# Optimization experiments

Hardware: AMD Instinct MI355X
Metric: run time of the kernel (lower is better)

## Reference

```python
import jax, jax.numpy as jnp
import numpy as np

N = 50000   # nodes
R = 3       # relations
E = 300000  # edges per relation
H, D = 4, 32  # heads, per-head dim (hidden_feat=128)
IN, HID, OUT = 128, 128, 64
SLOPE = 0.2  # DGL GATConv leaky_relu negative slope


def setup_inputs() -> dict:
    key = jax.random.key(0)
    ks = jax.random.split(key, 12)
    s = 0.05
    return {
        "x": jax.random.normal(ks[0], (N, IN), jnp.float32),
        "edges": jax.random.randint(ks[1], (R, 2, E), 0, N, jnp.int64),
        "W1": jax.random.normal(ks[2], (R, IN, H * D), jnp.float32) * s,
        "al1": jax.random.normal(ks[3], (R, H, D), jnp.float32) * s,
        "ar1": jax.random.normal(ks[4], (R, H, D), jnp.float32) * s,
        "b1": jnp.zeros((R, H, D), jnp.float32),
        "W2": jax.random.normal(ks[5], (R, HID, H * D), jnp.float32) * s,
        "al2": jax.random.normal(ks[6], (R, H, D), jnp.float32) * s,
        "ar2": jax.random.normal(ks[7], (R, H, D), jnp.float32) * s,
        "b2": jnp.zeros((R, H, D), jnp.float32),
        "Wl": jax.random.normal(ks[8], (HID, OUT), jnp.float32) * s,
        "bl": jnp.zeros((OUT,), jnp.float32),
    }


def rgat_layer(h, edges, W, al, ar, b):
    """HeteroGraphConv(sum) of per-relation GATConv. h: [N,F]. Returns [N,H,D]."""
    out = jnp.zeros((N, H, D), h.dtype)
    for r in range(R):  # small fixed relation count
        src, dst = edges[r, 0], edges[r, 1]
        feat = (h @ W[r]).reshape(N, H, D)                  # per-relation projection
        el = jnp.einsum("nhd,hd->nh", feat, al[r])          # [N,H]
        er = jnp.einsum("nhd,hd->nh", feat, ar[r])          # [N,H]
        e = jax.nn.leaky_relu(el[src] + er[dst], SLOPE)      # [E,H]
        # edge softmax over incoming edges per destination node
        emax = jax.ops.segment_max(e, dst, num_segments=N)   # [N,H]
        ex = jnp.exp(e - emax[dst])
        denom = jax.ops.segment_sum(ex, dst, num_segments=N) # [N,H]
        alpha = ex / denom[dst]                               # [E,H]
        msg = feat[src] * alpha[:, :, None]                   # [E,H,D]
        out = out + jax.ops.segment_sum(msg, dst, num_segments=N) + b[r]
    return out


def reference(x, edges, W1, al1, ar1, b1, W2, al2, ar2, b2, Wl, bl):
    h = rgat_layer(x, edges, W1, al1, ar1, b1).reshape(N, H * D)
    h = jax.nn.relu(h)  # dropout is identity in eval mode
    h = rgat_layer(h, edges, W2, al2, ar2, b2).reshape(N, H * D)
    return h @ Wl + bl  # [N, OUT]
```

## Files before the change

### kernel.cpp

```cpp
#include <hip/hip_runtime.h>
#include <hip/hip_bf16.h>
#include <hip/hip_fp16.h>
#include <type_traits>

#define Nn 50000
#define RR 3
#define EE 300000

typedef __attribute__((ext_vector_type(8))) short short8;
typedef __attribute__((ext_vector_type(4))) short short4v;
typedef __attribute__((ext_vector_type(4))) float floatx4;

__device__ __forceinline__ short f2bf(float f) {
    __hip_bfloat16 h = __float2bfloat16(f);
    return *reinterpret_cast<short*>(&h);
}


__global__ void count_wswz_kernel(const int* __restrict__ edges, int* __restrict__ counts,
                                  int* __restrict__ ord,
                                  const float* __restrict__ W1, const float* __restrict__ W2,
                                  short* __restrict__ Z) {
    int bx = blockIdx.x;
    if (bx >= 440) {
        int idx = (bx - 440) * 256 + threadIdx.x;
        if (idx >= 12288) return;
        int lane = idx & 63;
        int nt = (idx >> 6) & 7;
        int kt = (idx >> 9) & 3;
        int rl = idx >> 11;
        int layer = rl / 3, r = rl % 3;
        const float* W = (layer ? W2 : W1) + (size_t)r * 16384;
        int n = nt * 16 + (lane & 15);
        int k0 = kt * 32 + (lane >> 4) * 8;
        short8 v;
        #pragma unroll
        for (int j = 0; j < 8; ++j) v[j] = f2bf(W[(size_t)(k0 + j) * 128 + n]);
        *(short8*)&Z[(size_t)idx * 8] = v;
        return;
    }
    int i = bx * 256 + threadIdx.x;
    if (i >= RR * EE / 8) return;
    int g = i * 8;
    int r = g / EE, e0 = g - r * EE;
    const int* db = &edges[(size_t)r * 2 * EE + EE + e0];
    int4 d0 = *(const int4*)db;
    int4 d1 = *(const int4*)(db + 4);
    int* cb = counts + r * Nn;
    int4 o0, o1;
    o0.x = atomicAdd(&cb[d0.x], 1);
    o0.y = atomicAdd(&cb[d0.y], 1);
    o0.z = atomicAdd(&cb[d0.z], 1);
    o0.w = atomicAdd(&cb[d0.w], 1);
    o1.x = atomicAdd(&cb[d1.x], 1);
    o1.y = atomicAdd(&cb[d1.y], 1);
    o1.z = atomicAdd(&cb[d1.z], 1);
    o1.w = atomicAdd(&cb[d1.w], 1);
    *(int4*)&ord[g] = o0;
    *(int4*)&ord[g + 4] = o1;
}

__global__ __launch_bounds__(256) void alloc_kernel(const int* __restrict__ counts,
                                                    int* __restrict__ row_start,
                                                    int* __restrict__ totals) {
    __shared__ int s[256];
    __shared__ int base_s;
    int r = blockIdx.y;
    int tid = threadIdx.x;
    int n = blockIdx.x * 256 + tid;
    int idx = r * Nn + n;
    int c = (n < Nn) ? counts[idx] : 0;
    s[tid] = c;
    __syncthreads();
    #pragma unroll
    for (int off = 1; off < 256; off <<= 1) {
        int v = 0;
        if (tid >= off) v = s[tid - off];
        __syncthreads();
        if (tid >= off) s[tid] += v;
        __syncthreads();
    }
    if (tid == 255) base_s = atomicAdd(&totals[r], s[255]);
    __syncthreads();
    if (n < Nn) row_start[idx] = base_s + s[tid] - c;
}


__device__ __forceinline__ void scatter_body(int bid, const int* __restrict__ edges,
                                             const int* __restrict__ ord,
                                             const int* __restrict__ row_start,
                                             int* __restrict__ csr_s, int* __restrict__ csr_d) {
    int i = bid * 256 + threadIdx.x;
    if (i >= RR * EE / 8) return;
    int g = i * 8;
    int r = g / EE, e0 = g - r * EE;
    const int* sb = &edges[(size_t)r * 2 * EE + e0];
    const int* db = sb + EE;
    int4 s0 = *(const int4*)sb, s1 = *(const int4*)(sb + 4);
    int4 d0 = *(const int4*)db, d1 = *(const int4*)(db + 4);
    int4 o0 = *(const int4*)&ord[g], o1 = *(const int4*)&ord[g + 4];
    const int* rs = row_start + r * Nn;
    int* cs = csr_s + (size_t)r * EE;
    int* cd = csr_d + (size_t)r * EE;
    int p0 = rs[d0.x] + o0.x, p1 = rs[d0.y] + o0.y;
    int p2 = rs[d0.z] + o0.z, p3 = rs[d0.w] + o0.w;
    int p4 = rs[d1.x] + o1.x, p5 = rs[d1.y] + o1.y;
    int p6 = rs[d1.z] + o1.z, p7 = rs[d1.w] + o1.w;
    cs[p0] = s0.x; cs[p1] = s0.y; cs[p2] = s0.z; cs[p3] = s0.w;
    cs[p4] = s1.x; cs[p5] = s1.y; cs[p6] = s1.z; cs[p7] = s1.w;
    cd[p0] = d0.x; cd[p1] = d0.y; cd[p2] = d0.z; cd[p3] = d0.w;
    cd[p4] = d1.x; cd[p5] = d1.y; cd[p6] = d1.z; cd[p7] = d1.w;
}


template<typename TA, bool FUSE_SCATTER>
__global__ __launch_bounds__(256) void gemm_proj_mfma(const TA* __restrict__ A,
                                                      const short* __restrict__ Z,
                                                      const float* __restrict__ al,
                                                      const float* __restrict__ ar,
                                                      __half* __restrict__ C,
                                                      float* __restrict__ el,
                                                      float* __restrict__ er,
                                                      const int* __restrict__ edges,
                                                      const int* __restrict__ ord,
                                                      const int* __restrict__ row_start,
                                                      int* __restrict__ csr_s,
                                                      int* __restrict__ csr_d) {
    const int rowBlocks = (Nn + 63) / 64;
    if (FUSE_SCATTER && blockIdx.x >= rowBlocks) {
        scatter_body(blockIdx.x - rowBlocks, edges, ord, row_start, csr_s, csr_d);
        return;
    }
    __shared__ short A_lds[64 * 136];
    __shared__ float al_lds[384], ar_lds[384];
    int tid = threadIdx.x;
    int row0 = blockIdx.x * 64;
    if (tid < 128) { al_lds[256 + tid] = al[256 + tid]; ar_lds[256 + tid] = ar[256 + tid]; }
    al_lds[tid] = al[tid]; ar_lds[tid] = ar[tid];
    if constexpr (std::is_same<TA, float>::value) {
        #pragma unroll
        for (int p = 0; p < 8; ++p) {
            int f = p * 256 + tid;
            int row = f >> 5;
            int c4 = (f & 31) * 4;
            float4 v = make_float4(0.f, 0.f, 0.f, 0.f);
            if (row0 + row < Nn) v = *(const float4*)&A[(size_t)(row0 + row) * 128 + c4];
            short4v sv;
            sv[0] = f2bf(v.x); sv[1] = f2bf(v.y); sv[2] = f2bf(v.z); sv[3] = f2bf(v.w);
            *(short4v*)&A_lds[row * 136 + c4] = sv;
        }
    } else {
        #pragma unroll
        for (int p = 0; p < 4; ++p) {
            int c = p * 256 + tid;
            int row = c >> 4, c8 = (c & 15) * 8;
            short8 v = (short8)(0);
            if (row0 + row < Nn) v = *(const short8*)&A[(size_t)(row0 + row) * 128 + c8];
            *(short8*)&A_lds[row * 136 + c8] = v;
        }
    }
    __syncthreads();
    int wave = tid >> 6, lane = tid & 63;
    int m = lane & 15, q = lane >> 4;
    short8 af[4];
    #pragma unroll
    for (int kt = 0; kt < 4; ++kt)
        af[kt] = *(short8*)&A_lds[(wave * 16 + m) * 136 + kt * 32 + q * 8];
    __syncthreads();
    __half* lds_h = (__half*)A_lds;
    int row8 = tid >> 2;
    int hh = tid & 3;
    for (int r = 0; r < RR; ++r) {
        floatx4 acc[8];
        #pragma unroll
        for (int nt = 0; nt < 8; ++nt) acc[nt] = (floatx4)(0.f);
        const short* Zr = Z + (size_t)r * 16384;
        #pragma unroll
        for (int kt = 0; kt < 4; ++kt) {
            #pragma unroll
            for (int nt = 0; nt < 8; ++nt) {
                short8 bf = *(const short8*)&Zr[(size_t)(kt * 8 + nt) * 512 + lane * 8];
                acc[nt] = __builtin_amdgcn_mfma_f32_16x16x32_bf16(af[kt], bf, acc[nt], 0, 0, 0);
            }
        }
        #pragma unroll
        for (int nt = 0; nt < 8; ++nt) {
            int col = nt * 16 + m;
            #pragma unroll
            for (int reg = 0; reg < 4; ++reg)
                lds_h[(wave * 16 + q * 4 + reg) * 136 + col] = __float2half(acc[nt][reg]);
        }
        __syncthreads();
        __half* Cr = C + (size_t)r * Nn * 128;
        #pragma unroll
        for (int p = 0; p < 4; ++p) {
            int lin = p * 256 + tid;
            int row = lin >> 4, c8 = (lin & 15) * 8;
            if (row0 + row < Nn)
                *(short8*)&Cr[(size_t)(row0 + row) * 128 + c8] = *(short8*)&lds_h[row * 136 + c8];
        }
        {
            const __half2* fp = (const __half2*)&lds_h[row8 * 136 + hh * 32];
            const float* alp = &al_lds[r * 128 + hh * 32];
            const float* arp = &ar_lds[r * 128 + hh * 32];
            float sl = 0.f, sr = 0.f;
            #pragma unroll
            for (int d = 0; d < 16; ++d) {
                float2 v = __half22float2(fp[d]);
                sl += v.x * alp[2 * d] + v.y * alp[2 * d + 1];
                sr += v.x * arp[2 * d] + v.y * arp[2 * d + 1];
            }
            if (row0 + row8 < Nn) {
                size_t ei = (size_t)(r * Nn + row0 + row8) * 4 + hh;
                el[ei] = sl;
                er[ei] = sr;
            }
        }
        __syncthreads();
    }
}


__global__ __launch_bounds__(256) void gemm_final_kernel(const float* __restrict__ A,
                                                         const float* __restrict__ Wl,
                                                         const float* __restrict__ bl,
                                                         float* __restrict__ out) {
    __shared__ float As[16][65];
    __shared__ float Bs[16][65];
    int tid = threadIdx.x;
    int row0 = blockIdx.x * 64;
    float acc[4][4] = {};
    int tx = tid & 15, ty = tid >> 4;
    for (int k0 = 0; k0 < 128; k0 += 16) {
        {
            int mm = tid >> 2, c = (tid & 3) * 4;
            int row = row0 + mm;
            float4 v = make_float4(0.f, 0.f, 0.f, 0.f);
            if (row < Nn) v = *(const float4*)&A[(size_t)row * 128 + k0 + c];
            As[c + 0][mm] = v.x; As[c + 1][mm] = v.y; As[c + 2][mm] = v.z; As[c + 3][mm] = v.w;
        }
        {
            int kk = tid >> 4, j = (tid & 15) * 4;
            float4 v = *(const float4*)&Wl[(size_t)(k0 + kk) * 64 + j];
            *(float4*)&Bs[kk][j] = v;
        }
        __syncthreads();
        #pragma unroll
        for (int kk = 0; kk < 16; ++kk) {
            float4 a = *(const float4*)&As[kk][ty * 4];
            float4 b = *(const float4*)&Bs[kk][tx * 4];
            float av[4] = {a.x, a.y, a.z, a.w};
            float bv[4] = {b.x, b.y, b.z, b.w};
            #pragma unroll
            for (int i = 0; i < 4; ++i)
                #pragma unroll
                for (int j = 0; j < 4; ++j) acc[i][j] += av[i] * bv[j];
        }
        __syncthreads();
    }
    float4 bias = *(const float4*)&bl[tx * 4];
    #pragma unroll
    for (int i = 0; i < 4; ++i) {
        int row = row0 + ty * 4 + i;
        if (row >= Nn) continue;
        float4 v = make_float4(acc[i][0] + bias.x, acc[i][1] + bias.y,
                               acc[i][2] + bias.z, acc[i][3] + bias.w);
        *(float4*)&out[(size_t)row * 64 + tx * 4] = v;
    }
}


__global__ __launch_bounds__(256) void wexp_kernel(const int* __restrict__ csr_s,
                                                   const int* __restrict__ csr_d,
                                                   const float* __restrict__ el,
                                                   const float* __restrict__ er,
                                                   __half* __restrict__ wq) {
    int r = blockIdx.y;
    int k = blockIdx.x * 256 + threadIdx.x;
    if (k >= EE) return;
    size_t gk = (size_t)r * EE + k;
    int es = csr_s[gk], ed = csr_d[gk];
    float4 l4 = *(const float4*)&el[(size_t)(r * Nn + es) * 4];
    float4 r4 = *(const float4*)&er[(size_t)(r * Nn + ed) * 4];
    float lv[4] = {l4.x, l4.y, l4.z, l4.w};
    float rv[4] = {r4.x, r4.y, r4.z, r4.w};
    #pragma unroll
    for (int h = 0; h < 4; ++h) {
        float x = lv[h] + rv[h];
        x = (x > 0.f) ? x : 0.2f * x;
        wq[(size_t)h * (RR * EE) + gk] = __float2half(__expf(x));
    }
}


template<bool OUT_BF16_RELU>
__global__ __launch_bounds__(256) void agg_kernel(const __half2* __restrict__ feat2,
                                                  const __half* __restrict__ wq,
                                                  const int* __restrict__ csr_s,
                                                  const int* __restrict__ row_start,
                                                  const int* __restrict__ counts,
                                                  const float* __restrict__ b,
                                                  void* __restrict__ out) {
    int wave = threadIdx.x >> 6;
    int lane = threadIdx.x & 63;
    int n = blockIdx.x * 4 + wave;
    if (n >= Nn) return;
    int h = lane >> 4;
    int hl = lane & 15;
    int grp = lane & 48;
    int t2 = lane * 2;
    int cntA[RR], stA[RR], sC[RR];
    float wC[RR];
    #pragma unroll
    for (int r = 0; r < RR; ++r) {
        cntA[r] = counts[r * Nn + n];
        stA[r] = row_start[r * Nn + n];
    }
    #pragma unroll
    for (int r = 0; r < RR; ++r) {
        sC[r] = 0; wC[r] = 0.f;
        if (hl < cntA[r]) {
            int idx = stA[r] + hl;
            sC[r] = csr_s[(size_t)r * EE + idx];
            wC[r] = __half2float(wq[(size_t)h * (RR * EE) + (size_t)r * EE + idx]);
        }
    }
    float accx = b[t2] + b[128 + t2] + b[256 + t2];
    float accy = b[t2 + 1] + b[128 + t2 + 1] + b[256 + t2 + 1];
    #pragma unroll
    for (int r = 0; r < RR; ++r) {
        int cnt = cntA[r];
        if (cnt == 0) continue;
        const __half2* fr = feat2 + (size_t)r * Nn * 64;
        float den = 0.f, numx = 0.f, numy = 0.f;
        int s_l = sC[r];
        float w_l = wC[r];
        int i0 = 0;
        while (true) {
            int mm = cnt - i0; if (mm > 16) mm = 16;
            int mm8 = (mm + 7) & ~7;
            for (int j = 0; j < mm8; j += 8) {
                int s0 = __shfl(s_l, j);
                int s1 = __shfl(s_l, j + 1);
                int s2 = __shfl(s_l, j + 2);
                int s3 = __shfl(s_l, j + 3);
                int s4 = __shfl(s_l, j + 4);
                int s5 = __shfl(s_l, j + 5);
                int s6 = __shfl(s_l, j + 6);
                int s7 = __shfl(s_l, j + 7);
                float w0 = __shfl(w_l, grp | j);
                float w1 = __shfl(w_l, grp | (j + 1));
                float w2 = __shfl(w_l, grp | (j + 2));
                float w3 = __shfl(w_l, grp | (j + 3));
                float w4 = __shfl(w_l, grp | (j + 4));
                float w5 = __shfl(w_l, grp | (j + 5));
                float w6 = __shfl(w_l, grp | (j + 6));
                float w7 = __shfl(w_l, grp | (j + 7));
                __half2 f0 = fr[(size_t)s0 * 64 + lane];
                __half2 f1 = fr[(size_t)s1 * 64 + lane];
                __half2 f2 = fr[(size_t)s2 * 64 + lane];
                __half2 f3 = fr[(size_t)s3 * 64 + lane];
                __half2 f4 = fr[(size_t)s4 * 64 + lane];
                __half2 f5 = fr[(size_t)s5 * 64 + lane];
                __half2 f6 = fr[(size_t)s6 * 64 + lane];
                __half2 f7 = fr[(size_t)s7 * 64 + lane];
                float2 g0 = __half22float2(f0), g1 = __half22float2(f1);
                float2 g2 = __half22float2(f2), g3 = __half22float2(f3);
                float2 g4 = __half22float2(f4), g5 = __half22float2(f5);
                float2 g6 = __half22float2(f6), g7 = __half22float2(f7);
                den += ((w0 + w1) + (w2 + w3)) + ((w4 + w5) + (w6 + w7));
                numx += (w0 * g0.x + w1 * g1.x + w2 * g2.x + w3 * g3.x)
                      + (w4 * g4.x + w5 * g5.x + w6 * g6.x + w7 * g7.x);
                numy += (w0 * g0.y + w1 * g1.y + w2 * g2.y + w3 * g3.y)
                      + (w4 * g4.y + w5 * g5.y + w6 * g6.y + w7 * g7.y);
            }
            i0 += 16;
            if (i0 >= cnt) break;
            s_l = 0; w_l = 0.f;
            if (i0 + hl < cnt) {
                int idx = stA[r] + i0 + hl;
                s_l = csr_s[(size_t)r * EE + idx];
                w_l = __half2float(wq[(size_t)h * (RR * EE) + (size_t)r * EE + idx]);
            }
        }
        float inv = 1.f / den;
        accx += numx * inv;
        accy += numy * inv;
    }
    if constexpr (OUT_BF16_RELU) {
        short* o = (short*)out;
        short2 pk;
        pk.x = f2bf(fmaxf(accx, 0.f));
        pk.y = f2bf(fmaxf(accy, 0.f));
        *(short2*)&o[(size_t)n * 128 + t2] = pk;
    } else {
        float* o = (float*)out;
        *(float2*)&o[(size_t)n * 128 + t2] = make_float2(accx, accy);
    }
}


extern "C" void kernel_launch(void* const* d_in, const int* in_sizes, int n_in,
                              void* d_out, int out_size, void* d_ws, size_t ws_size,
                              hipStream_t stream) {
    const float* x   = (const float*)d_in[0];
    const int*  edges = (const int*)d_in[1];
    const float* W1  = (const float*)d_in[2];
    const float* al1 = (const float*)d_in[3];
    const float* ar1 = (const float*)d_in[4];
    const float* b1  = (const float*)d_in[5];
    const float* W2  = (const float*)d_in[6];
    const float* al2 = (const float*)d_in[7];
    const float* ar2 = (const float*)d_in[8];
    const float* b2  = (const float*)d_in[9];
    const float* Wl  = (const float*)d_in[10];
    const float* bl  = (const float*)d_in[11];
    float* out = (float*)d_out;

    __half* feat  = (__half*)d_ws;
    short* Z      = (short*)(feat + (size_t)RR * Nn * 128);
    float* el     = (float*)(Z + 98304);
    float* er     = el + (size_t)RR * Nn * 4;
    float* outbuf = er + (size_t)RR * Nn * 4;
    __half* wq    = (__half*)(outbuf + (size_t)Nn * 128);
    int* counts    = (int*)(wq + (size_t)4 * RR * EE);
    int* totals    = counts + RR * Nn;
    int* row_start = totals + 4;
    int* ord       = row_start + RR * Nn;
    int* csr_s     = ord + RR * EE;
    int* csr_d     = csr_s + RR * EE;
    short* outb16  = (short*)outbuf;

    const int rowBlocks  = (Nn + 63) / 64;
    const int nodeBlocks = (Nn + 255) / 256;
    const int aggBlocks  = (Nn + 3) / 4;
    const int edgeBlocks = (EE + 255) / 256;
    const int edge8Blocks = (RR * EE / 8 + 255) / 256;

    hipMemsetAsync(counts, 0, (size_t)(RR * Nn + 4) * sizeof(int), stream);
    count_wswz_kernel<<<440 + 48, 256, 0, stream>>>(edges, counts, ord, W1, W2, Z);
    alloc_kernel<<<dim3(nodeBlocks, RR), 256, 0, stream>>>(counts, row_start, totals);

    gemm_proj_mfma<float, true><<<rowBlocks + edge8Blocks, 256, 0, stream>>>(
        x, Z, al1, ar1, feat, el, er, edges, ord, row_start, csr_s, csr_d);
    wexp_kernel<<<dim3(edgeBlocks, RR), 256, 0, stream>>>(csr_s, csr_d, el, er, wq);
    agg_kernel<true><<<aggBlocks, 256, 0, stream>>>((const __half2*)feat, wq, csr_s, row_start, counts, b1, outb16);

    gemm_proj_mfma<short, false><<<rowBlocks, 256, 0, stream>>>(
        outb16, Z + 49152, al2, ar2, feat, el, er, nullptr, nullptr, nullptr, nullptr, nullptr);
    wexp_kernel<<<dim3(edgeBlocks, RR), 256, 0, stream>>>(csr_s, csr_d, el, er, wq);
    agg_kernel<false><<<aggBlocks, 256, 0, stream>>>((const __half2*)feat, wq, csr_s, row_start, counts, b2, outbuf);

    gemm_final_kernel<<<rowBlocks, 256, 0, stream>>>(outbuf, Wl, bl, out);
}
```

Measured before the change: 331.9 us.

## Pack source index with fp16 edge weight and interleave CSR src/dst

The edge-weight kernel now writes one 32-bit word per head and edge, holding the 16-bit source node index and the fp16 exp weight. The aggregation kernel can then fetch index and weight with a single load and a single shuffle instead of two. The CSR src/dst arrays are stored as interleaved int2 so the weight kernel reads both with one load. The CSR scatter is split out of the first projection GEMM into its own kernel, which adds a launch and removes the overlap with the GEMM. Packed weight storage doubles in size, and the packing relies on N fitting in 16 bits.

After: 333.5 us. No clear change (+0.5%).

```diff
diff --git a/kernel.cpp b/kernel.cpp
--- a/kernel.cpp
+++ b/kernel.cpp
@@ -85,12 +85,9 @@
     if (n < Nn) row_start[idx] = base_s + s[tid] - c;
 }
 
-
-__device__ __forceinline__ void scatter_body(int bid, const int* __restrict__ edges,
-                                             const int* __restrict__ ord,
-                                             const int* __restrict__ row_start,
-                                             int* __restrict__ csr_s, int* __restrict__ csr_d) {
-    int i = bid * 256 + threadIdx.x;
+__global__ void scatter_kernel(const int* __restrict__ edges, const int* __restrict__ ord,
+                               const int* __restrict__ row_start, int2* __restrict__ csr) {
+    int i = blockIdx.x * blockDim.x + threadIdx.x;
     if (i >= RR * EE / 8) return;
     int g = i * 8;
     int r = g / EE, e0 = g - r * EE;
@@ -100,37 +97,26 @@
     int4 d0 = *(const int4*)db, d1 = *(const int4*)(db + 4);
     int4 o0 = *(const int4*)&ord[g], o1 = *(const int4*)&ord[g + 4];
     const int* rs = row_start + r * Nn;
-    int* cs = csr_s + (size_t)r * EE;
-    int* cd = csr_d + (size_t)r * EE;
-    int p0 = rs[d0.x] + o0.x, p1 = rs[d0.y] + o0.y;
-    int p2 = rs[d0.z] + o0.z, p3 = rs[d0.w] + o0.w;
-    int p4 = rs[d1.x] + o1.x, p5 = rs[d1.y] + o1.y;
-    int p6 = rs[d1.z] + o1.z, p7 = rs[d1.w] + o1.w;
-    cs[p0] = s0.x; cs[p1] = s0.y; cs[p2] = s0.z; cs[p3] = s0.w;
-    cs[p4] = s1.x; cs[p5] = s1.y; cs[p6] = s1.z; cs[p7] = s1.w;
-    cd[p0] = d0.x; cd[p1] = d0.y; cd[p2] = d0.z; cd[p3] = d0.w;
-    cd[p4] = d1.x; cd[p5] = d1.y; cd[p6] = d1.z; cd[p7] = d1.w;
-}
-
-
-template<typename TA, bool FUSE_SCATTER>
+    int2* cb = csr + (size_t)r * EE;
+    cb[rs[d0.x] + o0.x] = make_int2(s0.x, d0.x);
+    cb[rs[d0.y] + o0.y] = make_int2(s0.y, d0.y);
+    cb[rs[d0.z] + o0.z] = make_int2(s0.z, d0.z);
+    cb[rs[d0.w] + o0.w] = make_int2(s0.w, d0.w);
+    cb[rs[d1.x] + o1.x] = make_int2(s1.x, d1.x);
+    cb[rs[d1.y] + o1.y] = make_int2(s1.y, d1.y);
+    cb[rs[d1.z] + o1.z] = make_int2(s1.z, d1.z);
+    cb[rs[d1.w] + o1.w] = make_int2(s1.w, d1.w);
+}
+
+
+template<typename TA>
 __global__ __launch_bounds__(256) void gemm_proj_mfma(const TA* __restrict__ A,
                                                       const short* __restrict__ Z,
                                                       const float* __restrict__ al,
                                                       const float* __restrict__ ar,
                                                       __half* __restrict__ C,
                                                       float* __restrict__ el,
-                                                      float* __restrict__ er,
-                                                      const int* __restrict__ edges,
-                                                      const int* __restrict__ ord,
-                                                      const int* __restrict__ row_start,
-                                                      int* __restrict__ csr_s,
-                                                      int* __restrict__ csr_d) {
-    const int rowBlocks = (Nn + 63) / 64;
-    if (FUSE_SCATTER && blockIdx.x >= rowBlocks) {
-        scatter_body(blockIdx.x - rowBlocks, edges, ord, row_start, csr_s, csr_d);
-        return;
-    }
+                                                      float* __restrict__ er) {
     __shared__ short A_lds[64 * 136];
     __shared__ float al_lds[384], ar_lds[384];
     int tid = threadIdx.x;
@@ -270,33 +256,33 @@
 }
 
 
-__global__ __launch_bounds__(256) void wexp_kernel(const int* __restrict__ csr_s,
-                                                   const int* __restrict__ csr_d,
+__global__ __launch_bounds__(256) void wexp_kernel(const int2* __restrict__ csr,
                                                    const float* __restrict__ el,
                                                    const float* __restrict__ er,
-                                                   __half* __restrict__ wq) {
+                                                   unsigned* __restrict__ wqp) {
     int r = blockIdx.y;
     int k = blockIdx.x * 256 + threadIdx.x;
     if (k >= EE) return;
     size_t gk = (size_t)r * EE + k;
-    int es = csr_s[gk], ed = csr_d[gk];
-    float4 l4 = *(const float4*)&el[(size_t)(r * Nn + es) * 4];
-    float4 r4 = *(const float4*)&er[(size_t)(r * Nn + ed) * 4];
+    int2 e = csr[gk];
+    float4 l4 = *(const float4*)&el[(size_t)(r * Nn + e.x) * 4];
+    float4 r4 = *(const float4*)&er[(size_t)(r * Nn + e.y) * 4];
     float lv[4] = {l4.x, l4.y, l4.z, l4.w};
     float rv[4] = {r4.x, r4.y, r4.z, r4.w};
+    unsigned sbits = (unsigned)e.x;
     #pragma unroll
     for (int h = 0; h < 4; ++h) {
         float x = lv[h] + rv[h];
         x = (x > 0.f) ? x : 0.2f * x;
-        wq[(size_t)h * (RR * EE) + gk] = __float2half(__expf(x));
+        unsigned wb = (unsigned)__half_as_ushort(__float2half(__expf(x)));
+        wqp[(size_t)h * (RR * EE) + gk] = sbits | (wb << 16);
     }
 }
 
 
 template<bool OUT_BF16_RELU>
 __global__ __launch_bounds__(256) void agg_kernel(const __half2* __restrict__ feat2,
-                                                  const __half* __restrict__ wq,
-                                                  const int* __restrict__ csr_s,
+                                                  const unsigned* __restrict__ wqp,
                                                   const int* __restrict__ row_start,
                                                   const int* __restrict__ counts,
                                                   const float* __restrict__ b,
@@ -309,8 +295,8 @@
     int hl = lane & 15;
     int grp = lane & 48;
     int t2 = lane * 2;
-    int cntA[RR], stA[RR], sC[RR];
-    float wC[RR];
+    int cntA[RR], stA[RR];
+    unsigned pC[RR];
     #pragma unroll
     for (int r = 0; r < RR; ++r) {
         cntA[r] = counts[r * Nn + n];
@@ -318,12 +304,9 @@
     }
     #pragma unroll
     for (int r = 0; r < RR; ++r) {
-        sC[r] = 0; wC[r] = 0.f;
-        if (hl < cntA[r]) {
-            int idx = stA[r] + hl;
-            sC[r] = csr_s[(size_t)r * EE + idx];
-            wC[r] = __half2float(wq[(size_t)h * (RR * EE) + (size_t)r * EE + idx]);
-        }
+        pC[r] = 0u;
+        if (hl < cntA[r])
+            pC[r] = wqp[(size_t)h * (RR * EE) + (size_t)r * EE + stA[r] + hl];
     }
     float accx = b[t2] + b[128 + t2] + b[256 + t2];
     float accy = b[t2 + 1] + b[128 + t2 + 1] + b[256 + t2 + 1];
@@ -333,37 +316,36 @@
         if (cnt == 0) continue;
         const __half2* fr = feat2 + (size_t)r * Nn * 64;
         float den = 0.f, numx = 0.f, numy = 0.f;
-        int s_l = sC[r];
-        float w_l = wC[r];
+        unsigned p_l = pC[r];
         int i0 = 0;
         while (true) {
             int mm = cnt - i0; if (mm > 16) mm = 16;
             int mm8 = (mm + 7) & ~7;
             for (int j = 0; j < mm8; j += 8) {
-                int s0 = __shfl(s_l, j);
-                int s1 = __shfl(s_l, j + 1);
-                int s2 = __shfl(s_l, j + 2);
-                int s3 = __shfl(s_l, j + 3);
-                int s4 = __shfl(s_l, j + 4);
-                int s5 = __shfl(s_l, j + 5);
-                int s6 = __shfl(s_l, j + 6);
-                int s7 = __shfl(s_l, j + 7);
-                float w0 = __shfl(w_l, grp | j);
-                float w1 = __shfl(w_l, grp | (j + 1));
-                float w2 = __shfl(w_l, grp | (j + 2));
-                float w3 = __shfl(w_l, grp | (j + 3));
-                float w4 = __shfl(w_l, grp | (j + 4));
-                float w5 = __shfl(w_l, grp | (j + 5));
-                float w6 = __shfl(w_l, grp | (j + 6));
-                float w7 = __shfl(w_l, grp | (j + 7));
-                __half2 f0 = fr[(size_t)s0 * 64 + lane];
-                __half2 f1 = fr[(size_t)s1 * 64 + lane];
-                __half2 f2 = fr[(size_t)s2 * 64 + lane];
-                __half2 f3 = fr[(size_t)s3 * 64 + lane];
-                __half2 f4 = fr[(size_t)s4 * 64 + lane];
-                __half2 f5 = fr[(size_t)s5 * 64 + lane];
-                __half2 f6 = fr[(size_t)s6 * 64 + lane];
-                __half2 f7 = fr[(size_t)s7 * 64 + lane];
+                unsigned u0 = __shfl(p_l, grp | j);
+                unsigned u1 = __shfl(p_l, grp | (j + 1));
+                unsigned u2 = __shfl(p_l, grp | (j + 2));
+                unsigned u3 = __shfl(p_l, grp | (j + 3));
+                unsigned u4 = __shfl(p_l, grp | (j + 4));
+                unsigned u5 = __shfl(p_l, grp | (j + 5));
+                unsigned u6 = __shfl(p_l, grp | (j + 6));
+                unsigned u7 = __shfl(p_l, grp | (j + 7));
+                __half2 f0 = fr[(size_t)(u0 & 0xFFFFu) * 64 + lane];
+                __half2 f1 = fr[(size_t)(u1 & 0xFFFFu) * 64 + lane];
+                __half2 f2 = fr[(size_t)(u2 & 0xFFFFu) * 64 + lane];
+                __half2 f3 = fr[(size_t)(u3 & 0xFFFFu) * 64 + lane];
+                __half2 f4 = fr[(size_t)(u4 & 0xFFFFu) * 64 + lane];
+                __half2 f5 = fr[(size_t)(u5 & 0xFFFFu) * 64 + lane];
+                __half2 f6 = fr[(size_t)(u6 & 0xFFFFu) * 64 + lane];
+                __half2 f7 = fr[(size_t)(u7 & 0xFFFFu) * 64 + lane];
+                float w0 = __half2float(__ushort_as_half((unsigned short)(u0 >> 16)));
+                float w1 = __half2float(__ushort_as_half((unsigned short)(u1 >> 16)));
+                float w2 = __half2float(__ushort_as_half((unsigned short)(u2 >> 16)));
+                float w3 = __half2float(__ushort_as_half((unsigned short)(u3 >> 16)));
+                float w4 = __half2float(__ushort_as_half((unsigned short)(u4 >> 16)));
+                float w5 = __half2float(__ushort_as_half((unsigned short)(u5 >> 16)));
+                float w6 = __half2float(__ushort_as_half((unsigned short)(u6 >> 16)));
+                float w7 = __half2float(__ushort_as_half((unsigned short)(u7 >> 16)));
                 float2 g0 = __half22float2(f0), g1 = __half22float2(f1);
                 float2 g2 = __half22float2(f2), g3 = __half22float2(f3);
                 float2 g4 = __half22float2(f4), g5 = __half22float2(f5);
@@ -376,12 +358,9 @@
             }
             i0 += 16;
             if (i0 >= cnt) break;
-            s_l = 0; w_l = 0.f;
-            if (i0 + hl < cnt) {
-                int idx = stA[r] + i0 + hl;
-                s_l = csr_s[(size_t)r * EE + idx];
-                w_l = __half2float(wq[(size_t)h * (RR * EE) + (size_t)r * EE + idx]);
-            }
+            p_l = 0u;
+            if (i0 + hl < cnt)
+                p_l = wqp[(size_t)h * (RR * EE) + (size_t)r * EE + stA[r] + i0 + hl];
         }
         float inv = 1.f / den;
         accx += numx * inv;
@@ -422,13 +401,12 @@
     float* el     = (float*)(Z + 98304);
     float* er     = el + (size_t)RR * Nn * 4;
     float* outbuf = er + (size_t)RR * Nn * 4;
-    __half* wq    = (__half*)(outbuf + (size_t)Nn * 128);
-    int* counts    = (int*)(wq + (size_t)4 * RR * EE);
+    unsigned* wqp = (unsigned*)(outbuf + (size_t)Nn * 128);
+    int* counts    = (int*)(wqp + (size_t)4 * RR * EE);
     int* totals    = counts + RR * Nn;
     int* row_start = totals + 4;
     int* ord       = row_start + RR * Nn;
-    int* csr_s     = ord + RR * EE;
-    int* csr_d     = csr_s + RR * EE;
+    int2* csr      = (int2*)(ord + RR * EE);
     short* outb16  = (short*)outbuf;
 
     const int rowBlocks  = (Nn + 63) / 64;
@@ -440,16 +418,15 @@
     hipMemsetAsync(counts, 0, (size_t)(RR * Nn + 4) * sizeof(int), stream);
     count_wswz_kernel<<<440 + 48, 256, 0, stream>>>(edges, counts, ord, W1, W2, Z);
     alloc_kernel<<<dim3(nodeBlocks, RR), 256, 0, stream>>>(counts, row_start, totals);
-
-    gemm_proj_mfma<float, true><<<rowBlocks + edge8Blocks, 256, 0, stream>>>(
-        x, Z, al1, ar1, feat, el, er, edges, ord, row_start, csr_s, csr_d);
-    wexp_kernel<<<dim3(edgeBlocks, RR), 256, 0, stream>>>(csr_s, csr_d, el, er, wq);
-    agg_kernel<true><<<aggBlocks, 256, 0, stream>>>((const __half2*)feat, wq, csr_s, row_start, counts, b1, outb16);
-
-    gemm_proj_mfma<short, false><<<rowBlocks, 256, 0, stream>>>(
-        outb16, Z + 49152, al2, ar2, feat, el, er, nullptr, nullptr, nullptr, nullptr, nullptr);
-    wexp_kernel<<<dim3(edgeBlocks, RR), 256, 0, stream>>>(csr_s, csr_d, el, er, wq);
-    agg_kernel<false><<<aggBlocks, 256, 0, stream>>>((const __half2*)feat, wq, csr_s, row_start, counts, b2, outbuf);
+    scatter_kernel<<<edge8Blocks, 256, 0, stream>>>(edges, ord, row_start, csr);
+
+    gemm_proj_mfma<float><<<rowBlocks, 256, 0, stream>>>(x, Z, al1, ar1, feat, el, er);
+    wexp_kernel<<<dim3(edgeBlocks, RR), 256, 0, stream>>>(csr, el, er, wqp);
+    agg_kernel<true><<<aggBlocks, 256, 0, stream>>>((const __half2*)feat, wqp, row_start, counts, b1, outb16);
+
+    gemm_proj_mfma<short><<<rowBlocks, 256, 0, stream>>>(outb16, Z + 49152, al2, ar2, feat, el, er);
+    wexp_kernel<<<dim3(edgeBlocks, RR), 256, 0, stream>>>(csr, el, er, wqp);
+    agg_kernel<false><<<aggBlocks, 256, 0, stream>>>((const __half2*)feat, wqp, row_start, counts, b2, outbuf);
 
     gemm_final_kernel<<<rowBlocks, 256, 0, stream>>>(outbuf, Wl, bl, out);
 }
```
